# Kernel optimization log

Measured on AMD Instinct MI355X. Metric: run time of the kernel, lower is better.

## Reference

```python
import jax, jax.numpy as jnp
import numpy as np
import math

D_MODEL = 256
N_HEADS = 4
WINDOW = 5
LN_EPS = 1e-5


def setup_inputs() -> dict:
    key = jax.random.key(0)
    ks = jax.random.split(key, 10)
    B, S, D = 8, 8192, D_MODEL
    s = 1.0 / math.sqrt(D)
    x = jax.random.normal(ks[0], (B, S, D), dtype=jnp.float32)
    Wq = jax.random.uniform(ks[1], (D, D), jnp.float32, -s, s)
    bq = jax.random.uniform(ks[2], (D,), jnp.float32, -s, s)
    Wk = jax.random.uniform(ks[3], (D, D), jnp.float32, -s, s)
    bk = jax.random.uniform(ks[4], (D,), jnp.float32, -s, s)
    Wv = jax.random.uniform(ks[5], (D, D), jnp.float32, -s, s)
    bv = jax.random.uniform(ks[6], (D,), jnp.float32, -s, s)
    Wo = jax.random.uniform(ks[7], (D, D), jnp.float32, -s, s)
    bo = jax.random.uniform(ks[8], (D,), jnp.float32, -s, s)
    gamma = jnp.ones((D,), jnp.float32)
    beta = jnp.zeros((D,), jnp.float32)
    return {"x": x, "Wq": Wq, "bq": bq, "Wk": Wk, "bk": bk,
            "Wv": Wv, "bv": bv, "Wo": Wo, "bo": bo,
            "gamma": gamma, "beta": beta}


def _layer_norm(y, gamma, beta):
    mu = jnp.mean(y, axis=-1, keepdims=True)
    var = jnp.mean(jnp.square(y - mu), axis=-1, keepdims=True)
    return (y - mu) * jax.lax.rsqrt(var + LN_EPS) * gamma + beta


def reference(x, Wq, bq, Wk, bk, Wv, bv, Wo, bo, gamma, beta):
    B, S, D = x.shape
    H, hd, W = N_HEADS, D // N_HEADS, WINDOW
    num_windows = (S + W - 1) // W
    pad_len = num_windows * W - S
    Sp = S + pad_len

    def proj(Wm, bm):
        # (B,S,D) -> (B,H,S,hd)
        p = (x @ Wm.T + bm).reshape(B, S, H, hd).transpose(0, 2, 1, 3)
        if pad_len > 0:
            p = jnp.pad(p, ((0, 0), (0, 0), (0, pad_len), (0, 0)))
        return p.reshape(B, H, num_windows, W, hd)

    Q = proj(Wq, bq)
    K = proj(Wk, bk)
    V = proj(Wv, bv)

    scores = jnp.einsum('bhnwd,bhnvd->bhnwv', Q, K) / math.sqrt(hd)
    attn = jax.nn.softmax(scores, axis=-1)  # dropout is identity in eval
    out = jnp.tanh(jnp.einsum('bhnwv,bhnvd->bhnwd', attn, V))

    out = out.reshape(B, H, Sp, hd)[:, :, :S, :]
    out = out.transpose(0, 2, 1, 3).reshape(B, S, D)
    out = out @ Wo.T + bo
    return _layer_norm(out + x, gamma, beta)
```

## Files before the change

kernel.cpp:

```cpp
#include <hip/hip_runtime.h>
#include <hip/hip_bf16.h>
#include <stdint.h>

typedef unsigned short u16;
typedef __attribute__((ext_vector_type(8))) __bf16 bf16x8;
typedef __attribute__((ext_vector_type(4))) float f32x4;

#define DEV static __device__ __forceinline__

DEV u16 f32_to_bf16(float f) {
  uint32_t u = __float_as_uint(f);
  u += 0x7fffu + ((u >> 16) & 1u);
  return (u16)(u >> 16);
}

DEV void unpack8(uint4 u, float* f) {
  uint32_t a[4] = {u.x, u.y, u.z, u.w};
#pragma unroll
  for (int i = 0; i < 4; ++i) {
    f[2 * i]     = __uint_as_float(a[i] << 16);
    f[2 * i + 1] = __uint_as_float(a[i] & 0xffff0000u);
  }
}

DEV uint4 pack8(const float* f) {
  uint32_t a[4];
#pragma unroll
  for (int i = 0; i < 4; ++i)
    a[i] = (uint32_t)f32_to_bf16(f[2 * i]) | ((uint32_t)f32_to_bf16(f[2 * i + 1]) << 16);
  return make_uint4(a[0], a[1], a[2], a[3]);
}

DEV void gload16(const u16* g, u16* l) {
  __builtin_amdgcn_global_load_lds(
      (const __attribute__((address_space(1))) void*)g,
      (__attribute__((address_space(3))) void*)l, 16, 0, 0);
}

__global__ __launch_bounds__(256) void convert_kernel(
    const float* __restrict__ x, const float* __restrict__ Wq,
    const float* __restrict__ Wk, const float* __restrict__ Wv,
    const float* __restrict__ Wo, u16* __restrict__ xb,
    u16* __restrict__ wqkv, u16* __restrict__ wob) {
  const size_t NX4 = (size_t)65536 * 256 / 4;
  size_t i = (size_t)blockIdx.x * 256 + threadIdx.x;
  const float* src;
  u16* dst;
  size_t off4;
  if (i < NX4) {
    src = x; dst = xb; off4 = i;
  } else {
    size_t w = i - NX4;
    int which = (int)(w >> 14);
    off4 = w & 16383;
    if (which == 0)      { src = Wq; dst = wqkv; }
    else if (which == 1) { src = Wk; dst = wqkv + 65536; }
    else if (which == 2) { src = Wv; dst = wqkv + 131072; }
    else                 { src = Wo; dst = wob; }
  }
  float4 v = reinterpret_cast<const float4*>(src)[off4];
  ushort4 o;
  o.x = f32_to_bf16(v.x); o.y = f32_to_bf16(v.y);
  o.z = f32_to_bf16(v.z); o.w = f32_to_bf16(v.w);
  reinterpret_cast<ushort4*>(dst)[off4] = o;
}

__global__ __launch_bounds__(256) void qkv_gemm3(
    const u16* __restrict__ Xb, const u16* __restrict__ Wqkv,
    const float* __restrict__ bq, const float* __restrict__ bk,
    const float* __restrict__ bv, u16* __restrict__ QKV) {
  __shared__ __align__(16) u16 As[128 * 32];
  __shared__ __align__(16) u16 Bs[128 * 32];
  const int bid = blockIdx.x;
  const int swz = (bid & 7) * 384 + (bid >> 3);
  const int bn = swz % 6;
  const int bm = swz / 6;
  const int tid = threadIdx.x;
  const int lane = tid & 63;
  const int wid = tid >> 6;
  const int wm = (wid >> 1) * 64;
  const int wn = (wid & 1) * 64;
  const int fr = lane & 15;
  const int fq = lane >> 4;

  const int c0 = tid, c1 = tid + 256;
  const int r0c = c0 >> 2, s0 = (c0 ^ (c0 >> 2)) & 3;
  const int r1c = c1 >> 2, s1 = (c1 ^ (c1 >> 2)) & 3;
  const u16* Ag0 = Xb + (size_t)(bm * 128 + r0c) * 256 + s0 * 8;
  const u16* Ag1 = Xb + (size_t)(bm * 128 + r1c) * 256 + s1 * 8;
  const u16* Bg0 = Wqkv + (size_t)(bn * 128 + r0c) * 256 + s0 * 8;
  const u16* Bg1 = Wqkv + (size_t)(bn * 128 + r1c) * 256 + s1 * 8;
  u16* lA0 = As + c0 * 8;
  u16* lA1 = As + c1 * 8;
  u16* lB0 = Bs + c0 * 8;
  u16* lB1 = Bs + c1 * 8;

  f32x4 acc[4][4] = {};

  for (int kt = 0; kt < 8; ++kt) {
    gload16(Ag0 + kt * 32, lA0);
    gload16(Ag1 + kt * 32, lA1);
    gload16(Bg0 + kt * 32, lB0);
    gload16(Bg1 + kt * 32, lB1);
    __syncthreads();
    bf16x8 af[4], bf[4];
#pragma unroll
    for (int m = 0; m < 4; ++m) {
      int row = wm + m * 16 + fr;
      af[m] = *reinterpret_cast<const bf16x8*>(As + row * 32 + ((fq ^ (row & 3)) * 8));
    }
#pragma unroll
    for (int n = 0; n < 4; ++n) {
      int row = wn + n * 16 + fr;
      bf[n] = *reinterpret_cast<const bf16x8*>(Bs + row * 32 + ((fq ^ (row & 3)) * 8));
    }
#pragma unroll
    for (int m = 0; m < 4; ++m)
#pragma unroll
      for (int n = 0; n < 4; ++n)
        acc[m][n] = __builtin_amdgcn_mfma_f32_16x16x32_bf16(af[m], bf[n], acc[m][n], 0, 0, 0);
    __syncthreads();
  }

  const float* bias = (bn < 2) ? (bq + (bn & 1) * 128)
                    : (bn < 4) ? (bk + ((bn - 2) & 1) * 128)
                               : (bv + ((bn - 4) & 1) * 128);
  float bv4[4];
#pragma unroll
  for (int n = 0; n < 4; ++n) bv4[n] = bias[wn + n * 16 + fr];

#pragma unroll
  for (int m = 0; m < 4; ++m)
#pragma unroll
    for (int r = 0; r < 4; ++r) {
      int row = bm * 128 + wm + m * 16 + fq * 4 + r;
      u16* orow = QKV + (size_t)row * 768 + bn * 128;
#pragma unroll
      for (int n = 0; n < 4; ++n)
        orow[wn + n * 16 + fr] = f32_to_bf16(acc[m][n][r] + bv4[n]);
    }
}

__global__ __launch_bounds__(256) void attn_kernel(const u16* __restrict__ QKV,
                                                   u16* __restrict__ AO) {
  const int S = 8192, NW = 1639, CH = 205;
  int wgid = blockIdx.x * 4 + (threadIdx.x >> 6);
  int lane = threadIdx.x & 63;
  int b = wgid / (4 * CH);
  int rm = wgid % (4 * CH);
  int h = rm / CH;
  int ch = rm % CH;
  int w = ch * 8 + (lane >> 3);
  int t = lane & 7;
  bool wv = (w < NW);

  float kv[5][8], vv[5][8];
#pragma unroll
  for (int j = 0; j < 5; ++j) {
    int s = w * 5 + j;
    if (wv && s < S) {
      size_t off = ((size_t)b * S + s) * 768 + h * 64 + t * 8;
      unpack8(*reinterpret_cast<const uint4*>(QKV + off + 256), kv[j]);
      unpack8(*reinterpret_cast<const uint4*>(QKV + off + 512), vv[j]);
    } else {
#pragma unroll
      for (int d = 0; d < 8; ++d) { kv[j][d] = 0.f; vv[j][d] = 0.f; }
    }
  }

#pragma unroll
  for (int i = 0; i < 5; ++i) {
    int s = w * 5 + i;
    bool sv = wv && (s < S);
    float q[8];
    if (sv) {
      size_t off = ((size_t)b * S + s) * 768 + h * 64 + t * 8;
      unpack8(*reinterpret_cast<const uint4*>(QKV + off), q);
    } else {
#pragma unroll
      for (int d = 0; d < 8; ++d) q[d] = 0.f;
    }
    float sc[5];
#pragma unroll
    for (int j = 0; j < 5; ++j) {
      float p = 0.f;
#pragma unroll
      for (int d = 0; d < 8; ++d) p += q[d] * kv[j][d];
      sc[j] = p;
    }
#pragma unroll
    for (int mask = 1; mask <= 4; mask <<= 1)
#pragma unroll
      for (int j = 0; j < 5; ++j) sc[j] += __shfl_xor(sc[j], mask);
#pragma unroll
    for (int j = 0; j < 5; ++j) sc[j] *= 0.125f;
    float mx = sc[0];
#pragma unroll
    for (int j = 1; j < 5; ++j) mx = fmaxf(mx, sc[j]);
    float e[5], sum = 0.f;
#pragma unroll
    for (int j = 0; j < 5; ++j) { e[j] = __expf(sc[j] - mx); sum += e[j]; }
    float inv = 1.0f / sum;
    float o[8];
#pragma unroll
    for (int d = 0; d < 8; ++d) {
      float a = 0.f;
#pragma unroll
      for (int j = 0; j < 5; ++j) a += e[j] * vv[j][d];
      float v2 = a * inv;
      float e2 = __expf(2.0f * v2);
      o[d] = 1.0f - 2.0f / (e2 + 1.0f);
    }
    if (sv) {
      size_t oo = ((size_t)b * S + s) * 256 + h * 64 + t * 8;
      *reinterpret_cast<uint4*>(AO + oo) = pack8(o);
    }
  }
}

__global__ __launch_bounds__(256) void o_gemm_ln3(
    const u16* __restrict__ AO, const u16* __restrict__ Wob,
    const float* __restrict__ bo, const float* __restrict__ x,
    const float* __restrict__ gamma, const float* __restrict__ beta,
    float* __restrict__ out) {
  __shared__ __align__(16) u16 As[64 * 32];
  __shared__ __align__(16) u16 Bs[256 * 32];
  __shared__ float pS[4][64], pQ[4][64], muS[64], rsS[64];
  const int bm = blockIdx.x;
  const int tid = threadIdx.x;
  const int lane = tid & 63;
  const int wid = tid >> 6;
  const int wn = wid * 64;
  const int fr = lane & 15;
  const int fq = lane >> 4;
  const int row0 = bm * 64;

  const int ra = tid >> 2, sa = (tid ^ (tid >> 2)) & 3;
  const u16* Ag = AO + (size_t)(row0 + ra) * 256 + sa * 8;
  u16* lA = As + tid * 8;
  const u16* Bg0 = Wob + (size_t)((tid) >> 2) * 256 + (((tid) ^ ((tid) >> 2)) & 3) * 8;
  const u16* Bg1 = Wob + (size_t)((tid + 256) >> 2) * 256 + (((tid + 256) ^ ((tid + 256) >> 2)) & 3) * 8;
  const u16* Bg2 = Wob + (size_t)((tid + 512) >> 2) * 256 + (((tid + 512) ^ ((tid + 512) >> 2)) & 3) * 8;
  const u16* Bg3 = Wob + (size_t)((tid + 768) >> 2) * 256 + (((tid + 768) ^ ((tid + 768) >> 2)) & 3) * 8;
  u16* lB0 = Bs + tid * 8;
  u16* lB1 = Bs + (tid + 256) * 8;
  u16* lB2 = Bs + (tid + 512) * 8;
  u16* lB3 = Bs + (tid + 768) * 8;

  f32x4 acc[4][4] = {};

  for (int kt = 0; kt < 8; ++kt) {
    gload16(Ag + kt * 32, lA);
    gload16(Bg0 + kt * 32, lB0);
    gload16(Bg1 + kt * 32, lB1);
    gload16(Bg2 + kt * 32, lB2);
    gload16(Bg3 + kt * 32, lB3);
    __syncthreads();
    bf16x8 af[4], bf[4];
#pragma unroll
    for (int m = 0; m < 4; ++m) {
      int row = m * 16 + fr;
      af[m] = *reinterpret_cast<const bf16x8*>(As + row * 32 + ((fq ^ (row & 3)) * 8));
    }
#pragma unroll
    for (int n = 0; n < 4; ++n) {
      int row = wn + n * 16 + fr;
      bf[n] = *reinterpret_cast<const bf16x8*>(Bs + row * 32 + ((fq ^ (row & 3)) * 8));
    }
#pragma unroll
    for (int m = 0; m < 4; ++m)
#pragma unroll
      for (int n = 0; n < 4; ++n)
        acc[m][n] = __builtin_amdgcn_mfma_f32_16x16x32_bf16(af[m], bf[n], acc[m][n], 0, 0, 0);
    __syncthreads();
  }

  float bov[4], gv[4], bev[4];
#pragma unroll
  for (int n = 0; n < 4; ++n) {
    int c = wn + n * 16 + fr;
    bov[n] = bo[c]; gv[n] = gamma[c]; bev[n] = beta[c];
  }
#pragma unroll
  for (int m = 0; m < 4; ++m)
#pragma unroll
    for (int r = 0; r < 4; ++r) {
      size_t rg = (size_t)(row0 + m * 16 + fq * 4 + r);
#pragma unroll
      for (int n = 0; n < 4; ++n)
        acc[m][n][r] += bov[n] + x[rg * 256 + wn + n * 16 + fr];
    }

#pragma unroll
  for (int m = 0; m < 4; ++m)
#pragma unroll
    for (int r = 0; r < 4; ++r) {
      float s1 = 0.f, s2 = 0.f;
#pragma unroll
      for (int n = 0; n < 4; ++n) {
        float vx = acc[m][n][r];
        s1 += vx; s2 += vx * vx;
      }
#pragma unroll
      for (int mask = 1; mask <= 8; mask <<= 1) {
        s1 += __shfl_xor(s1, mask);
        s2 += __shfl_xor(s2, mask);
      }
      if (fr == 0) {
        int row = m * 16 + fq * 4 + r;
        pS[wid][row] = s1; pQ[wid][row] = s2;
      }
    }
  __syncthreads();
  if (tid < 64) {
    float s1 = pS[0][tid] + pS[1][tid] + pS[2][tid] + pS[3][tid];
    float s2 = pQ[0][tid] + pQ[1][tid] + pQ[2][tid] + pQ[3][tid];
    float mu = s1 * (1.0f / 256.0f);
    float var = s2 * (1.0f / 256.0f) - mu * mu;
    muS[tid] = mu;
    rsS[tid] = rsqrtf(var + 1e-5f);
  }
  __syncthreads();
#pragma unroll
  for (int m = 0; m < 4; ++m)
#pragma unroll
    for (int r = 0; r < 4; ++r) {
      int row = m * 16 + fq * 4 + r;
      float mu = muS[row], rs = rsS[row];
      float* orow = out + (size_t)(row0 + row) * 256;
#pragma unroll
      for (int n = 0; n < 4; ++n)
        orow[wn + n * 16 + fr] = (acc[m][n][r] - mu) * rs * gv[n] + bev[n];
    }
}

extern "C" void kernel_launch(void* const* d_in, const int* in_sizes, int n_in,
                              void* d_out, int out_size, void* d_ws, size_t ws_size,
                              hipStream_t stream) {
  const float* x     = (const float*)d_in[0];
  const float* Wq    = (const float*)d_in[1];
  const float* bq    = (const float*)d_in[2];
  const float* Wk    = (const float*)d_in[3];
  const float* bk    = (const float*)d_in[4];
  const float* Wv    = (const float*)d_in[5];
  const float* bv    = (const float*)d_in[6];
  const float* Wo    = (const float*)d_in[7];
  const float* bo    = (const float*)d_in[8];
  const float* gamma = (const float*)d_in[9];
  const float* beta  = (const float*)d_in[10];
  float* out = (float*)d_out;

  char* ws = (char*)d_ws;
  u16* xb   = (u16*)(ws);
  u16* wqkv = (u16*)(ws + 33554432);
  u16* wob  = (u16*)(ws + 33947648);
  u16* qkv  = (u16*)(ws + 34078720);
  u16* ao   = (u16*)(ws + 134742016);

  convert_kernel<<<16640, 256, 0, stream>>>(x, Wq, Wk, Wv, Wo, xb, wqkv, wob);
  qkv_gemm3<<<3072, 256, 0, stream>>>(xb, wqkv, bq, bk, bv, qkv);
  attn_kernel<<<1640, 256, 0, stream>>>(qkv, ao);
  o_gemm_ln3<<<1024, 256, 0, stream>>>(ao, wob, bo, x, gamma, beta, out);
}
```

Baseline: 236.8 us.

## Fuse window attention into O-projection+LayerNorm kernel and double-buffer QKV GEMM

The attention kernel is merged into the output-projection/LayerNorm kernel. Each block computes attention for 16 windows (80 rows) across all heads and writes results to a swizzled LDS tile, which the MFMA GEMM then consumes directly. This removes the global write and re-read of the attention output. The QKV GEMM and the Wo tiles now use double-buffered LDS so the next K-slice load overlaps compute. The cost is higher LDS use and fewer, heavier blocks, which may reduce occupancy and latency hiding.

```diff
diff --git a/kernel.cpp b/kernel.cpp
--- a/kernel.cpp
+++ b/kernel.cpp
@@ -65,12 +65,12 @@
   reinterpret_cast<ushort4*>(dst)[off4] = o;
 }
 
-__global__ __launch_bounds__(256) void qkv_gemm3(
+__global__ __launch_bounds__(256) void qkv_gemm4(
     const u16* __restrict__ Xb, const u16* __restrict__ Wqkv,
     const float* __restrict__ bq, const float* __restrict__ bk,
     const float* __restrict__ bv, u16* __restrict__ QKV) {
-  __shared__ __align__(16) u16 As[128 * 32];
-  __shared__ __align__(16) u16 Bs[128 * 32];
+  __shared__ __align__(16) u16 As[2][128 * 32];
+  __shared__ __align__(16) u16 Bs[2][128 * 32];
   const int bid = blockIdx.x;
   const int swz = (bid & 7) * 384 + (bid >> 3);
   const int bn = swz % 6;
@@ -90,29 +90,34 @@
   const u16* Ag1 = Xb + (size_t)(bm * 128 + r1c) * 256 + s1 * 8;
   const u16* Bg0 = Wqkv + (size_t)(bn * 128 + r0c) * 256 + s0 * 8;
   const u16* Bg1 = Wqkv + (size_t)(bn * 128 + r1c) * 256 + s1 * 8;
-  u16* lA0 = As + c0 * 8;
-  u16* lA1 = As + c1 * 8;
-  u16* lB0 = Bs + c0 * 8;
-  u16* lB1 = Bs + c1 * 8;
 
   f32x4 acc[4][4] = {};
 
+  gload16(Ag0, &As[0][c0 * 8]);
+  gload16(Ag1, &As[0][c1 * 8]);
+  gload16(Bg0, &Bs[0][c0 * 8]);
+  gload16(Bg1, &Bs[0][c1 * 8]);
+  __syncthreads();
+
   for (int kt = 0; kt < 8; ++kt) {
-    gload16(Ag0 + kt * 32, lA0);
-    gload16(Ag1 + kt * 32, lA1);
-    gload16(Bg0 + kt * 32, lB0);
-    gload16(Bg1 + kt * 32, lB1);
-    __syncthreads();
+    const int cur = kt & 1;
+    if (kt < 7) {
+      const int nxt = cur ^ 1;
+      gload16(Ag0 + (kt + 1) * 32, &As[nxt][c0 * 8]);
+      gload16(Ag1 + (kt + 1) * 32, &As[nxt][c1 * 8]);
+      gload16(Bg0 + (kt + 1) * 32, &Bs[nxt][c0 * 8]);
+      gload16(Bg1 + (kt + 1) * 32, &Bs[nxt][c1 * 8]);
+    }
     bf16x8 af[4], bf[4];
 #pragma unroll
     for (int m = 0; m < 4; ++m) {
       int row = wm + m * 16 + fr;
-      af[m] = *reinterpret_cast<const bf16x8*>(As + row * 32 + ((fq ^ (row & 3)) * 8));
+      af[m] = *reinterpret_cast<const bf16x8*>(&As[cur][row * 32 + ((fq ^ (row & 3)) * 8)]);
     }
 #pragma unroll
     for (int n = 0; n < 4; ++n) {
       int row = wn + n * 16 + fr;
-      bf[n] = *reinterpret_cast<const bf16x8*>(Bs + row * 32 + ((fq ^ (row & 3)) * 8));
+      bf[n] = *reinterpret_cast<const bf16x8*>(&Bs[cur][row * 32 + ((fq ^ (row & 3)) * 8)]);
     }
 #pragma unroll
     for (int m = 0; m < 4; ++m)
@@ -141,134 +146,138 @@
     }
 }
 
-__global__ __launch_bounds__(256) void attn_kernel(const u16* __restrict__ QKV,
-                                                   u16* __restrict__ AO) {
-  const int S = 8192, NW = 1639, CH = 205;
-  int wgid = blockIdx.x * 4 + (threadIdx.x >> 6);
-  int lane = threadIdx.x & 63;
-  int b = wgid / (4 * CH);
-  int rm = wgid % (4 * CH);
-  int h = rm / CH;
-  int ch = rm % CH;
-  int w = ch * 8 + (lane >> 3);
-  int t = lane & 7;
-  bool wv = (w < NW);
-
-  float kv[5][8], vv[5][8];
-#pragma unroll
-  for (int j = 0; j < 5; ++j) {
-    int s = w * 5 + j;
-    if (wv && s < S) {
-      size_t off = ((size_t)b * S + s) * 768 + h * 64 + t * 8;
-      unpack8(*reinterpret_cast<const uint4*>(QKV + off + 256), kv[j]);
-      unpack8(*reinterpret_cast<const uint4*>(QKV + off + 512), vv[j]);
-    } else {
-#pragma unroll
-      for (int d = 0; d < 8; ++d) { kv[j][d] = 0.f; vv[j][d] = 0.f; }
-    }
-  }
-
-#pragma unroll
-  for (int i = 0; i < 5; ++i) {
-    int s = w * 5 + i;
-    bool sv = wv && (s < S);
-    float q[8];
-    if (sv) {
-      size_t off = ((size_t)b * S + s) * 768 + h * 64 + t * 8;
-      unpack8(*reinterpret_cast<const uint4*>(QKV + off), q);
-    } else {
-#pragma unroll
-      for (int d = 0; d < 8; ++d) q[d] = 0.f;
-    }
-    float sc[5];
-#pragma unroll
-    for (int j = 0; j < 5; ++j) {
-      float p = 0.f;
-#pragma unroll
-      for (int d = 0; d < 8; ++d) p += q[d] * kv[j][d];
-      sc[j] = p;
-    }
-#pragma unroll
-    for (int mask = 1; mask <= 4; mask <<= 1)
-#pragma unroll
-      for (int j = 0; j < 5; ++j) sc[j] += __shfl_xor(sc[j], mask);
-#pragma unroll
-    for (int j = 0; j < 5; ++j) sc[j] *= 0.125f;
-    float mx = sc[0];
-#pragma unroll
-    for (int j = 1; j < 5; ++j) mx = fmaxf(mx, sc[j]);
-    float e[5], sum = 0.f;
-#pragma unroll
-    for (int j = 0; j < 5; ++j) { e[j] = __expf(sc[j] - mx); sum += e[j]; }
-    float inv = 1.0f / sum;
-    float o[8];
-#pragma unroll
-    for (int d = 0; d < 8; ++d) {
-      float a = 0.f;
-#pragma unroll
-      for (int j = 0; j < 5; ++j) a += e[j] * vv[j][d];
-      float v2 = a * inv;
-      float e2 = __expf(2.0f * v2);
-      o[d] = 1.0f - 2.0f / (e2 + 1.0f);
-    }
-    if (sv) {
-      size_t oo = ((size_t)b * S + s) * 256 + h * 64 + t * 8;
-      *reinterpret_cast<uint4*>(AO + oo) = pack8(o);
-    }
-  }
-}
-
-__global__ __launch_bounds__(256) void o_gemm_ln3(
-    const u16* __restrict__ AO, const u16* __restrict__ Wob,
+__global__ __launch_bounds__(256) void attn_o_ln(
+    const u16* __restrict__ QKV, const u16* __restrict__ Wob,
     const float* __restrict__ bo, const float* __restrict__ x,
     const float* __restrict__ gamma, const float* __restrict__ beta,
     float* __restrict__ out) {
-  __shared__ __align__(16) u16 As[64 * 32];
-  __shared__ __align__(16) u16 Bs[256 * 32];
-  __shared__ float pS[4][64], pQ[4][64], muS[64], rsS[64];
-  const int bm = blockIdx.x;
+  __shared__ __align__(16) u16 AOs[80 * 256];
+  __shared__ __align__(16) u16 Bs[2][256 * 32];
+  __shared__ float pS[4][80], pQ[4][80], muS[80], rsS[80];
+  const int S = 8192, NW = 1639;
+  const int bb = blockIdx.x;
+  const int b = bb / 103;
+  const int blk = bb % 103;
+  const int row0 = blk * 80;
   const int tid = threadIdx.x;
   const int lane = tid & 63;
   const int wid = tid >> 6;
-  const int wn = wid * 64;
   const int fr = lane & 15;
   const int fq = lane >> 4;
-  const int row0 = bm * 64;
-
-  const int ra = tid >> 2, sa = (tid ^ (tid >> 2)) & 3;
-  const u16* Ag = AO + (size_t)(row0 + ra) * 256 + sa * 8;
-  u16* lA = As + tid * 8;
-  const u16* Bg0 = Wob + (size_t)((tid) >> 2) * 256 + (((tid) ^ ((tid) >> 2)) & 3) * 8;
-  const u16* Bg1 = Wob + (size_t)((tid + 256) >> 2) * 256 + (((tid + 256) ^ ((tid + 256) >> 2)) & 3) * 8;
-  const u16* Bg2 = Wob + (size_t)((tid + 512) >> 2) * 256 + (((tid + 512) ^ ((tid + 512) >> 2)) & 3) * 8;
-  const u16* Bg3 = Wob + (size_t)((tid + 768) >> 2) * 256 + (((tid + 768) ^ ((tid + 768) >> 2)) & 3) * 8;
-  u16* lB0 = Bs + tid * 8;
-  u16* lB1 = Bs + (tid + 256) * 8;
-  u16* lB2 = Bs + (tid + 512) * 8;
-  u16* lB3 = Bs + (tid + 768) * 8;
-
-  f32x4 acc[4][4] = {};
+
+  const int t = tid & 7;
+#pragma unroll
+  for (int p = 0; p < 2; ++p) {
+    int pair = (tid >> 3) + p * 32;
+    int wloc = pair >> 2;
+    int h = pair & 3;
+    int w = blk * 16 + wloc;
+    bool wv = (w < NW);
+
+    float kv[5][8], vv[5][8];
+#pragma unroll
+    for (int j = 0; j < 5; ++j) {
+      int s = w * 5 + j;
+      if (wv && s < S) {
+        size_t off = ((size_t)b * S + s) * 768 + h * 64 + t * 8;
+        unpack8(*reinterpret_cast<const uint4*>(QKV + off + 256), kv[j]);
+        unpack8(*reinterpret_cast<const uint4*>(QKV + off + 512), vv[j]);
+      } else {
+#pragma unroll
+        for (int d = 0; d < 8; ++d) { kv[j][d] = 0.f; vv[j][d] = 0.f; }
+      }
+    }
+
+#pragma unroll
+    for (int i = 0; i < 5; ++i) {
+      int s = w * 5 + i;
+      bool sv = wv && (s < S);
+      float q[8];
+      if (sv) {
+        size_t off = ((size_t)b * S + s) * 768 + h * 64 + t * 8;
+        unpack8(*reinterpret_cast<const uint4*>(QKV + off), q);
+      } else {
+#pragma unroll
+        for (int d = 0; d < 8; ++d) q[d] = 0.f;
+      }
+      float sc[5];
+#pragma unroll
+      for (int j = 0; j < 5; ++j) {
+        float pp = 0.f;
+#pragma unroll
+        for (int d = 0; d < 8; ++d) pp += q[d] * kv[j][d];
+        sc[j] = pp;
+      }
+#pragma unroll
+      for (int mask = 1; mask <= 4; mask <<= 1)
+#pragma unroll
+        for (int j = 0; j < 5; ++j) sc[j] += __shfl_xor(sc[j], mask);
+#pragma unroll
+      for (int j = 0; j < 5; ++j) sc[j] *= 0.125f;
+      float mx = sc[0];
+#pragma unroll
+      for (int j = 1; j < 5; ++j) mx = fmaxf(mx, sc[j]);
+      float e[5], sum = 0.f;
+#pragma unroll
+      for (int j = 0; j < 5; ++j) { e[j] = __expf(sc[j] - mx); sum += e[j]; }
+      float inv = 1.0f / sum;
+      float o[8];
+#pragma unroll
+      for (int d = 0; d < 8; ++d) {
+        float a = 0.f;
+#pragma unroll
+        for (int j = 0; j < 5; ++j) a += e[j] * vv[j][d];
+        float v2 = a * inv;
+        float e2 = __expf(2.0f * v2);
+        o[d] = 1.0f - 2.0f / (e2 + 1.0f);
+      }
+      if (sv) {
+        int rl = wloc * 5 + i;
+        int chk = (h * 8 + t) ^ (rl & 7);
+        *reinterpret_cast<uint4*>(&AOs[rl * 256 + chk * 8]) = pack8(o);
+      }
+    }
+  }
+  __syncthreads();
+
+  const u16* Bg[4];
+#pragma unroll
+  for (int j = 0; j < 4; ++j) {
+    int c = tid + j * 256;
+    Bg[j] = Wob + (size_t)(c >> 2) * 256 + ((c ^ (c >> 2)) & 3) * 8;
+  }
+  gload16(Bg[0], &Bs[0][(tid) * 8]);
+  gload16(Bg[1], &Bs[0][(tid + 256) * 8]);
+  gload16(Bg[2], &Bs[0][(tid + 512) * 8]);
+  gload16(Bg[3], &Bs[0][(tid + 768) * 8]);
+  __syncthreads();
+
+  const int wn = wid * 64;
+  f32x4 acc[5][4] = {};
 
   for (int kt = 0; kt < 8; ++kt) {
-    gload16(Ag + kt * 32, lA);
-    gload16(Bg0 + kt * 32, lB0);
-    gload16(Bg1 + kt * 32, lB1);
-    gload16(Bg2 + kt * 32, lB2);
-    gload16(Bg3 + kt * 32, lB3);
-    __syncthreads();
-    bf16x8 af[4], bf[4];
-#pragma unroll
-    for (int m = 0; m < 4; ++m) {
+    const int cur = kt & 1;
+    if (kt < 7) {
+      const int nxt = cur ^ 1;
+      gload16(Bg[0] + (kt + 1) * 32, &Bs[nxt][(tid) * 8]);
+      gload16(Bg[1] + (kt + 1) * 32, &Bs[nxt][(tid + 256) * 8]);
+      gload16(Bg[2] + (kt + 1) * 32, &Bs[nxt][(tid + 512) * 8]);
+      gload16(Bg[3] + (kt + 1) * 32, &Bs[nxt][(tid + 768) * 8]);
+    }
+    bf16x8 af[5], bf[4];
+#pragma unroll
+    for (int m = 0; m < 5; ++m) {
       int row = m * 16 + fr;
-      af[m] = *reinterpret_cast<const bf16x8*>(As + row * 32 + ((fq ^ (row & 3)) * 8));
+      int chk = (kt * 4 + fq) ^ (row & 7);
+      af[m] = *reinterpret_cast<const bf16x8*>(&AOs[row * 256 + chk * 8]);
     }
 #pragma unroll
     for (int n = 0; n < 4; ++n) {
       int row = wn + n * 16 + fr;
-      bf[n] = *reinterpret_cast<const bf16x8*>(Bs + row * 32 + ((fq ^ (row & 3)) * 8));
-    }
-#pragma unroll
-    for (int m = 0; m < 4; ++m)
+      bf[n] = *reinterpret_cast<const bf16x8*>(&Bs[cur][row * 32 + ((fq ^ (row & 3)) * 8)]);
+    }
+#pragma unroll
+    for (int m = 0; m < 5; ++m)
 #pragma unroll
       for (int n = 0; n < 4; ++n)
         acc[m][n] = __builtin_amdgcn_mfma_f32_16x16x32_bf16(af[m], bf[n], acc[m][n], 0, 0, 0);
@@ -282,17 +291,20 @@
     bov[n] = bo[c]; gv[n] = gamma[c]; bev[n] = beta[c];
   }
 #pragma unroll
-  for (int m = 0; m < 4; ++m)
+  for (int m = 0; m < 5; ++m)
 #pragma unroll
     for (int r = 0; r < 4; ++r) {
-      size_t rg = (size_t)(row0 + m * 16 + fq * 4 + r);
-#pragma unroll
-      for (int n = 0; n < 4; ++n)
-        acc[m][n][r] += bov[n] + x[rg * 256 + wn + n * 16 + fr];
-    }
-
-#pragma unroll
-  for (int m = 0; m < 4; ++m)
+      int rl = m * 16 + fq * 4 + r;
+      if (row0 + rl < S) {
+        size_t rg = (size_t)b * S + row0 + rl;
+#pragma unroll
+        for (int n = 0; n < 4; ++n)
+          acc[m][n][r] += bov[n] + x[rg * 256 + wn + n * 16 + fr];
+      }
+    }
+
+#pragma unroll
+  for (int m = 0; m < 5; ++m)
 #pragma unroll
     for (int r = 0; r < 4; ++r) {
       float s1 = 0.f, s2 = 0.f;
@@ -307,12 +319,12 @@
         s2 += __shfl_xor(s2, mask);
       }
       if (fr == 0) {
-        int row = m * 16 + fq * 4 + r;
-        pS[wid][row] = s1; pQ[wid][row] = s2;
-      }
-    }
-  __syncthreads();
-  if (tid < 64) {
+        int rl = m * 16 + fq * 4 + r;
+        pS[wid][rl] = s1; pQ[wid][rl] = s2;
+      }
+    }
+  __syncthreads();
+  if (tid < 80) {
     float s1 = pS[0][tid] + pS[1][tid] + pS[2][tid] + pS[3][tid];
     float s2 = pQ[0][tid] + pQ[1][tid] + pQ[2][tid] + pQ[3][tid];
     float mu = s1 * (1.0f / 256.0f);
@@ -322,15 +334,17 @@
   }
   __syncthreads();
 #pragma unroll
-  for (int m = 0; m < 4; ++m)
+  for (int m = 0; m < 5; ++m)
 #pragma unroll
     for (int r = 0; r < 4; ++r) {
-      int row = m * 16 + fq * 4 + r;
-      float mu = muS[row], rs = rsS[row];
-      float* orow = out + (size_t)(row0 + row) * 256;
-#pragma unroll
-      for (int n = 0; n < 4; ++n)
-        orow[wn + n * 16 + fr] = (acc[m][n][r] - mu) * rs * gv[n] + bev[n];
+      int rl = m * 16 + fq * 4 + r;
+      if (row0 + rl < S) {
+        float mu = muS[rl], rs = rsS[rl];
+        float* orow = out + ((size_t)b * S + row0 + rl) * 256;
+#pragma unroll
+        for (int n = 0; n < 4; ++n)
+          orow[wn + n * 16 + fr] = (acc[m][n][r] - mu) * rs * gv[n] + bev[n];
+      }
     }
 }
 
@@ -355,10 +369,8 @@
   u16* wqkv = (u16*)(ws + 33554432);
   u16* wob  = (u16*)(ws + 33947648);
   u16* qkv  = (u16*)(ws + 34078720);
-  u16* ao   = (u16*)(ws + 134742016);
 
   convert_kernel<<<16640, 256, 0, stream>>>(x, Wq, Wk, Wv, Wo, xb, wqkv, wob);
-  qkv_gemm3<<<3072, 256, 0, stream>>>(xb, wqkv, bq, bk, bv, qkv);
-  attn_kernel<<<1640, 256, 0, stream>>>(qkv, ao);
-  o_gemm_ln3<<<1024, 256, 0, stream>>>(ao, wob, bo, x, gamma, beta, out);
-}
+  qkv_gemm4<<<3072, 256, 0, stream>>>(xb, wqkv, bq, bk, bv, qkv);
+  attn_o_ln<<<824, 256, 0, stream>>>(qkv, wob, bo, x, gamma, beta, out);
+}
```

Result: slower. 290.7 us (+22.8%).
